# Kernel optimization log

Measured on AMD Instinct MI355X. Metric: run time of the kernel, lower is better.

## Reference

```python
import jax, jax.numpy as jnp
import numpy as np

B, T, D = 64, 512, 256
K = 8192  # num_embeddings


def setup_inputs() -> dict:
    key = jax.random.key(0)
    k1, k2 = jax.random.split(key)
    inputs = jax.random.normal(k1, (B, T, D), dtype=jnp.float32)
    # nn.Embedding weight init: uniform(-1/K, 1/K)
    emb_weight = jax.random.uniform(k2, (K, D), dtype=jnp.float32, minval=-1.0 / K, maxval=1.0 / K)
    return {"inputs": inputs, "emb_weight": emb_weight}


def reference(inputs, emb_weight):
    d = emb_weight.shape[1]
    flat = inputs.reshape(-1, d)  # [N, D]
    # squared L2 distances to all codes: [N, K]
    distances = (
        jnp.sum(flat * flat, axis=1, keepdims=True)
        + jnp.sum(emb_weight * emb_weight, axis=1)
        - 2.0 * jnp.matmul(flat, emb_weight.T)
    )
    encoding_indices = jnp.argmin(distances, axis=1)  # [N]
    # one-hot @ codebook == direct gather of nearest code
    quantized = emb_weight[encoding_indices].reshape(inputs.shape)
    e_latent_loss = jnp.mean((jax.lax.stop_gradient(quantized) - inputs) ** 2)
    q_latent_loss = jnp.mean((quantized - jax.lax.stop_gradient(inputs)) ** 2)
    loss = q_latent_loss + e_latent_loss
    # straight-through estimator
    quantized_st = inputs + jax.lax.stop_gradient(quantized - inputs)
    return quantized_st, loss, encoding_indices.reshape(inputs.shape[0], -1)
```

## Files before the change

kernel.cpp:

```cpp
#include <hip/hip_runtime.h>

#define N_ROWS 32768
#define DIM 256
#define N_CODES 8192
#define OUT_Q 8388608
#define OUT_LOSS 8388608
#define OUT_IDX 8388609
#define FLAG_GAP 7e-5f
#define GAP3 1e-4f
#define CAND_CAP 262144

#define WS_AROW 0
#define WS_IDX  131072
#define WS_LIST 262144
#define WS_CNT  393216
#define WS_S1   393472
#define WS_KEYS 524544
#define WS_PART 524544
#define WS_EIMG 1048576

typedef __attribute__((ext_vector_type(8))) short short8x;
typedef __attribute__((ext_vector_type(4))) float f32x4;
typedef unsigned long long u64;
#define AS1 __attribute__((address_space(1)))
#define AS3 __attribute__((address_space(3)))

__device__ __forceinline__ u64 umin64(u64 a, u64 b) { return a < b ? a : b; }
__device__ __forceinline__ unsigned fkey(float f) {
    unsigned b = __float_as_uint(f);
    return b ^ (unsigned)(((int)b >> 31) | 0x80000000);
}
__device__ __forceinline__ float fkeyinv(unsigned u) {
    unsigned b = (u >> 31) ? (u ^ 0x80000000u) : ~u;
    return __uint_as_float(b);
}
__device__ __forceinline__ unsigned short bf16rne(float f) {
    unsigned u = __float_as_uint(f);
    return (unsigned short)((u + 0x7fff + ((u >> 16) & 1)) >> 16);
}
__device__ __forceinline__ void gload16(const void* g, void* l) {
    __builtin_amdgcn_global_load_lds((const AS1 unsigned int*)g, (AS3 unsigned int*)l, 16, 0, 0);
}
__device__ __forceinline__ void triple_merge(u64& k1, u64& k2, u64& k3, u64 o1, u64 o2, u64 o3) {
    bool c = o1 < k1;
    u64 A1 = c ? o1 : k1, A2 = c ? o2 : k2, A3 = c ? o3 : k3;
    u64 B1 = c ? k1 : o1, B2 = c ? k2 : o2;
    bool d = B1 < A2;
    k1 = A1;
    k2 = d ? B1 : A2;
    k3 = d ? umin64(A2, B2) : umin64(A3, B1);
}

__global__ void vq_prepE(const float* __restrict__ E, char* __restrict__ Eimg) {
    int t = blockIdx.x * 256 + threadIdx.x;
    int cb = t >> 10;
    int u = t & 1023;
    int w = u >> 7, v = u & 127;
    int sub = v >> 5, c = (v >> 4) & 1, l15 = v & 15;
    int tile = cb >> 3, S = cb & 7;
    const float* src = E + (size_t)(tile * 256 + w * 32 + c * 16 + l15) * DIM + S * 32 + sub * 8;
    unsigned short h[8], l[8];
#pragma unroll
    for (int j = 0; j < 8; ++j) {
        float vv = src[j];
        h[j] = bf16rne(vv);
        float hf = __uint_as_float((unsigned)h[j] << 16);
        l[j] = bf16rne(vv - hf);
    }
    short8x H, L;
#pragma unroll
    for (int j = 0; j < 8; ++j) { H[j] = (short)h[j]; L[j] = (short)l[j]; }
    char* dst = Eimg + (size_t)cb * 32768 + w * 4096 + sub * 512 + c * 256 + l15 * 16;
    *(short8x*)dst = H;
    *(short8x*)(dst + 2048) = L;
}

__global__ void vq_rowA(const float* __restrict__ X, float* __restrict__ Arow) {
    int row = blockIdx.x * 4 + (threadIdx.x >> 6);
    int lane = threadIdx.x & 63;
    const float4 v = *((const float4*)(X + (size_t)row * DIM + lane * 4));
    double s = (double)v.x * v.x + (double)v.y * v.y + (double)v.z * v.z + (double)v.w * v.w;
#pragma unroll
    for (int m = 1; m < 64; m <<= 1) s += __shfl_xor(s, m, 64);
    if (lane == 0) Arow[row] = (float)s;
}

template <int MODE>
__global__ __launch_bounds__(512, 1) void vq_scan(
    const float* __restrict__ X, const char* __restrict__ Eimg,
    const float* __restrict__ Arow, int* __restrict__ ws_idx,
    int* __restrict__ flaglist, int* __restrict__ flagcnt,
    u64* __restrict__ keybuf, float* __restrict__ s1buf,
    unsigned* __restrict__ cand, int* __restrict__ candcnt,
    int* __restrict__ list2, int* __restrict__ cnt2) {
    __shared__ alignas(16) unsigned short Xs[32768];
    __shared__ alignas(16) unsigned short Eb[32768];
    __shared__ int rows_s[64];

    const int tid = threadIdx.x;
    const int lane = tid & 63, wv = tid >> 6;
    const int l15 = lane & 15, sub = lane >> 4;

    const int cnt = (MODE == 1) ? *flagcnt : 0;
    const int ntasks = (MODE == 1) ? ((cnt + 63) >> 6) * 16 : 0;

    char* const ebase = (char*)Eb + wv * 4096;
    const char* const eimgw = Eimg + wv * 4096;

    float r1v[4][4], r2v[4][4], r3v[4][4];
    int c1v[4][4], c2v[4][4];
    if constexpr (MODE == 0) {
#pragma unroll
        for (int f = 0; f < 4; ++f)
#pragma unroll
            for (int g = 0; g < 4; ++g) {
                r1v[f][g] = 3.4e38f; r2v[f][g] = 3.4e38f; r3v[f][g] = 3.4e38f;
                c1v[f][g] = 0; c2v[f][g] = 0;
            }
    }

    int task = blockIdx.x;
    while (true) {
        int t0, t1, r0;
        if constexpr (MODE == 1) {
            if (task >= ntasks) break;
            int grp = task >> 4;
            int rng = task & 15;
            t0 = rng * 2; t1 = t0 + 2;
            r0 = 0;
            __syncthreads();
            if (tid < 64) {
                int s = grp * 64 + tid;
                rows_s[tid] = flaglist[s < cnt ? s : cnt - 1];
            }
            __syncthreads();
        } else {
            t0 = 0; t1 = 32;
            r0 = blockIdx.x * 64;
        }
        const int cend = t1 * 8;

        {
            const int ci = t0 * 8;
            const char* src = eimgw + (size_t)ci * 32768 + lane * 16;
            char* dst = ebase + (ci & 1) * 32768;
#pragma unroll
            for (int i = 0; i < 4; ++i) gload16(src + i * 1024, dst + i * 1024);
        }
#pragma unroll
        for (int i = 0; i < 4; ++i) {
            int ci = tid + i * 512;
            int q = ci >> 6, r = ci & 63;
            int grow = (MODE == 1) ? rows_s[r] : r0 + r;
            const float* src = X + (size_t)grow * DIM + q * 8;
            unsigned short h[8], l[8];
#pragma unroll
            for (int j = 0; j < 8; ++j) {
                float v = src[j];
                h[j] = bf16rne(v);
                float hf = __uint_as_float((unsigned)h[j] << 16);
                l[j] = bf16rne(v - hf);
            }
            short8x H, L;
#pragma unroll
            for (int j = 0; j < 8; ++j) { H[j] = (short)h[j]; L[j] = (short)l[j]; }
            *(short8x*)((char*)Xs + q * 1024 + r * 16) = H;
            *(short8x*)((char*)Xs + 32768 + q * 1024 + r * 16) = L;
        }

        float A_r[4][4], s1v[4][4];
        int rid[4][4];
#pragma unroll
        for (int f = 0; f < 4; ++f)
#pragma unroll
            for (int g = 0; g < 4; ++g) {
                int rr = (MODE == 1) ? rows_s[f * 16 + sub * 4 + g] : r0 + f * 16 + sub * 4 + g;
                A_r[f][g] = Arow[rr];
                if constexpr (MODE == 1) { s1v[f][g] = s1buf[rr]; rid[f][g] = rr; }
            }

        __syncthreads();

        for (int t = t0; t < t1; ++t) {
            f32x4 acc[4][2];
#pragma unroll
            for (int f = 0; f < 4; ++f)
#pragma unroll
                for (int c = 0; c < 2; ++c) acc[f][c] = (f32x4){0.f, 0.f, 0.f, 0.f};

#pragma unroll
            for (int S = 0; S < 8; ++S) {
                const int ci = t * 8 + S;
                if (ci + 1 < cend) {
                    const char* src = eimgw + (size_t)(ci + 1) * 32768 + lane * 16;
                    char* dst = ebase + ((ci + 1) & 1) * 32768;
#pragma unroll
                    for (int i = 0; i < 4; ++i) gload16(src + i * 1024, dst + i * 1024);
                    __builtin_amdgcn_sched_barrier(0);
                    asm volatile("s_waitcnt vmcnt(4)" ::: "memory");
                } else {
                    asm volatile("s_waitcnt vmcnt(0)" ::: "memory");
                }
                __builtin_amdgcn_sched_barrier(0);

                const char* xb = (const char*)Xs;
                const char* eb = ebase + (ci & 1) * 32768;
                short8x ah[4], al[4], ehh[2], ell[2];
#pragma unroll
                for (int f = 0; f < 4; ++f) {
                    int off = (S * 4 + sub) * 1024 + f * 256 + l15 * 16;
                    ah[f] = *(const short8x*)(xb + off);
                    al[f] = *(const short8x*)(xb + 32768 + off);
                }
#pragma unroll
                for (int c = 0; c < 2; ++c) {
                    int off = sub * 512 + c * 256 + l15 * 16;
                    ehh[c] = *(const short8x*)(eb + off);
                    ell[c] = *(const short8x*)(eb + 2048 + off);
                }
#pragma unroll
                for (int f = 0; f < 4; ++f)
#pragma unroll
                    for (int c = 0; c < 2; ++c) {
                        f32x4 a = acc[f][c];
                        a = __builtin_amdgcn_mfma_f32_16x16x32_bf16(al[f], ehh[c], a, 0, 0, 0);
                        a = __builtin_amdgcn_mfma_f32_16x16x32_bf16(ah[f], ell[c], a, 0, 0, 0);
                        a = __builtin_amdgcn_mfma_f32_16x16x32_bf16(ah[f], ehh[c], a, 0, 0, 0);
                        acc[f][c] = a;
                    }
            }

            const int cbase = t * 256 + wv * 32 + l15;
            if constexpr (MODE == 0) {
#pragma unroll
                for (int f = 0; f < 4; ++f)
#pragma unroll
                    for (int g = 0; g < 4; ++g) {
                        float v0 = fmaf(-2.0f, acc[f][0][g], A_r[f][g]);
                        float v1 = fmaf(-2.0f, acc[f][1][g], A_r[f][g]);
                        bool sw = v1 < v0;
                        float lo = sw ? v1 : v0, hi = sw ? v0 : v1;
                        int ilo = sw ? cbase + 16 : cbase;
                        int ihi = sw ? cbase : cbase + 16;
                        bool cond = lo < r1v[f][g];
                        float A2 = cond ? hi : r2v[f][g];
                        float A3 = cond ? 3.4e38f : r3v[f][g];
                        float B1 = cond ? r1v[f][g] : lo;
                        float B2 = cond ? r2v[f][g] : hi;
                        int iA2 = cond ? ihi : c2v[f][g];
                        int iB1 = cond ? c1v[f][g] : ilo;
                        r1v[f][g] = cond ? lo : r1v[f][g];
                        c1v[f][g] = cond ? ilo : c1v[f][g];
                        bool d = B1 < A2;
                        r2v[f][g] = d ? B1 : A2;
                        c2v[f][g] = d ? iB1 : iA2;
                        r3v[f][g] = d ? fminf(A2, B2) : fminf(A3, B1);
                    }
            } else {
#pragma unroll
                for (int f = 0; f < 4; ++f)
#pragma unroll
                    for (int g = 0; g < 4; ++g) {
                        float thr = s1v[f][g] + FLAG_GAP;
#pragma unroll
                        for (int c = 0; c < 2; ++c) {
                            float v = fmaf(-2.0f, acc[f][c][g], A_r[f][g]);
                            if (v <= thr) {
                                int slot = atomicAdd(candcnt, 1);
                                if (slot < CAND_CAP)
                                    cand[slot] = ((unsigned)rid[f][g] << 13) |
                                                 (unsigned)(cbase + c * 16);
                            }
                        }
                    }
            }
        }

        if constexpr (MODE == 0) break;
        else task += gridDim.x;
    }

    if constexpr (MODE == 0) {
        __syncthreads();
        u64* red = (u64*)Xs;
#pragma unroll
        for (int f = 0; f < 4; ++f)
#pragma unroll
            for (int g = 0; g < 4; ++g) {
                u64 k1 = ((u64)fkey(r1v[f][g]) << 32) | (unsigned)c1v[f][g];
                u64 k2 = ((u64)fkey(r2v[f][g]) << 32) | (unsigned)c2v[f][g];
                u64 k3 = ((u64)fkey(r3v[f][g]) << 32) | 0x1fffu;
#pragma unroll
                for (int m = 1; m < 16; m <<= 1) {
                    u64 o1 = __shfl_xor(k1, m, 64);
                    u64 o2 = __shfl_xor(k2, m, 64);
                    u64 o3 = __shfl_xor(k3, m, 64);
                    triple_merge(k1, k2, k3, o1, o2, o3);
                }
                if (l15 == 0) {
                    int row64 = f * 16 + sub * 4 + g;
                    red[(wv * 64 + row64) * 3 + 0] = k1;
                    red[(wv * 64 + row64) * 3 + 1] = k2;
                    red[(wv * 64 + row64) * 3 + 2] = k3;
                }
            }
        __syncthreads();
        if (tid < 64) {
            u64 K1 = red[tid * 3 + 0], K2 = red[tid * 3 + 1], K3 = red[tid * 3 + 2];
#pragma unroll
            for (int w = 1; w < 8; ++w) {
                triple_merge(K1, K2, K3,
                             red[(w * 64 + tid) * 3 + 0],
                             red[(w * 64 + tid) * 3 + 1],
                             red[(w * 64 + tid) * 3 + 2]);
            }
            int r = blockIdx.x * 64 + tid;
            ws_idx[r] = (int)(unsigned)(K1 & 0xffffffffull);
            float s1 = fkeyinv((unsigned)(K1 >> 32));
            float s2 = fkeyinv((unsigned)(K2 >> 32));
            float s3 = fkeyinv((unsigned)(K3 >> 32));
            s1buf[r] = s1;
            if (s2 - s1 < FLAG_GAP) {
                keybuf[r] = ~0ull;
                flaglist[atomicAdd(flagcnt, 1)] = r;
                int cs = atomicAdd(candcnt, 2);
                if (cs + 1 < CAND_CAP) {
                    cand[cs]     = ((unsigned)r << 13) | (unsigned)(K1 & 8191ull);
                    cand[cs + 1] = ((unsigned)r << 13) | (unsigned)(K2 & 8191ull);
                }
                if (s3 - s1 <= GAP3) list2[atomicAdd(cnt2, 1)] = r;
            }
        }
    }
}

__global__ void vq_refine_cand(const float* __restrict__ X, const float* __restrict__ E,
                               const float* __restrict__ Arow, u64* __restrict__ keybuf,
                               const unsigned* __restrict__ cand,
                               const int* __restrict__ candcnt) {
    int cnt2 = *candcnt;
    cnt2 = cnt2 < CAND_CAP ? cnt2 : CAND_CAP;
    const int gw = (blockIdx.x * 256 + threadIdx.x) >> 6;
    const int nw = gridDim.x * 4;
    const int lane = threadIdx.x & 63;
    for (int i = gw; i < cnt2; i += nw) {
        unsigned p = cand[i];
        int row = (int)(p >> 13), code = (int)(p & 8191);
        float4 xv = *(const float4*)(X + (size_t)row * DIM + lane * 4);
        float4 ev = *(const float4*)(E + (size_t)code * DIM + lane * 4);
        double s = (double)xv.x * ev.x + (double)xv.y * ev.y +
                   (double)xv.z * ev.z + (double)xv.w * ev.w;
#pragma unroll
        for (int m = 1; m < 64; m <<= 1) s += __shfl_xor(s, m, 64);
        if (lane == 0) {
            float m32 = (float)s;
            float scr = fmaf(-2.0f, m32, Arow[row]);
            u64 key = ((u64)fkey(scr) << 32) | (unsigned)code;
            atomicMin(keybuf + row, key);
        }
    }
}

__global__ void vq_apply(const u64* __restrict__ keybuf, const int* __restrict__ flaglist,
                         const int* __restrict__ flagcnt, int* __restrict__ ws_idx) {
    int s = blockIdx.x * 256 + threadIdx.x;
    if (s < *flagcnt) {
        int r = flaglist[s];
        u64 k = keybuf[r];
        if (k != ~0ull) ws_idx[r] = (int)(unsigned)(k & 0xffffffffull);
    }
}

__global__ void vq_out(const float* __restrict__ X, const float* __restrict__ E,
                       const int* __restrict__ ws_idx, float* __restrict__ out,
                       float* __restrict__ partials) {
    const int r = (blockIdx.x * 256 + threadIdx.x) >> 6;
    const int lane = threadIdx.x & 63;
    int idx = ws_idx[r];
    idx = idx < 0 ? 0 : (idx > N_CODES - 1 ? N_CODES - 1 : idx);
    float4 e = *((const float4*)(E + (size_t)idx * DIM + lane * 4));
    float4 x = *((const float4*)(X + (size_t)r * DIM + lane * 4));
    float dx = e.x - x.x, dy = e.y - x.y, dz = e.z - x.z, dw = e.w - x.w;
    float4 o;
    o.x = x.x + dx; o.y = x.y + dy; o.z = x.z + dz; o.w = x.w + dw;
    *((float4*)(out + (size_t)r * DIM + lane * 4)) = o;
    float s = dx * dx + dy * dy + dz * dz + dw * dw;
#pragma unroll
    for (int m = 1; m < 64; m <<= 1) s += __shfl_xor(s, m, 64);
    if (lane == 0) {
        partials[r] = s;
        out[OUT_IDX + r] = (float)idx;
    }
}

__global__ void vq_loss(const float* __restrict__ partials, float* __restrict__ out) {
    __shared__ double sred[4];
    double s = 0.0;
    for (int i = threadIdx.x; i < N_ROWS; i += 256) s += (double)partials[i];
#pragma unroll
    for (int m = 1; m < 64; m <<= 1) s += __shfl_xor(s, m, 64);
    if ((threadIdx.x & 63) == 0) sred[threadIdx.x >> 6] = s;
    __syncthreads();
    if (threadIdx.x == 0) {
        double t = sred[0] + sred[1] + sred[2] + sred[3];
        out[OUT_LOSS] = (float)(2.0 * t / (double)OUT_Q);
    }
}

extern "C" void kernel_launch(void* const* d_in, const int* in_sizes, int n_in,
                              void* d_out, int out_size, void* d_ws, size_t ws_size,
                              hipStream_t stream) {
    const float* X = (const float*)d_in[0];
    const float* E = (const float*)d_in[1];
    float* out = (float*)d_out;
    char* ws = (char*)d_ws;

    float* Arow = (float*)(ws + WS_AROW);
    int* idx = (int*)(ws + WS_IDX);
    int* list = (int*)(ws + WS_LIST);
    int* cnt = (int*)(ws + WS_CNT);
    int* cnt2 = (int*)(ws + WS_CNT + 8);
    int* ccnt = (int*)(ws + WS_CNT + 16);
    float* s1buf = (float*)(ws + WS_S1);
    u64* keys = (u64*)(ws + WS_KEYS);
    float* part = (float*)(ws + WS_PART);
    char* eimg = (ws_size >= (size_t)(WS_EIMG + 8 * 1024 * 1024)) ? (ws + WS_EIMG) : (char*)d_out;
    unsigned* cand = (unsigned*)((char*)d_out + (16 << 20));
    int* list2 = (int*)((char*)d_out + (17 << 20));

    hipMemsetAsync(ws + WS_CNT, 0, 32, stream);
    vq_prepE<<<1024, 256, 0, stream>>>(E, eimg);
    vq_rowA<<<N_ROWS / 4, 256, 0, stream>>>(X, Arow);
    vq_scan<0><<<N_ROWS / 64, 512, 0, stream>>>(X, eimg, Arow, idx, list, cnt, keys, s1buf,
                                                cand, ccnt, list2, cnt2);
    vq_scan<1><<<512, 512, 0, stream>>>(X, eimg, Arow, idx, list2, cnt2, keys, s1buf,
                                        cand, ccnt, list2, cnt2);
    vq_refine_cand<<<1024, 256, 0, stream>>>(X, E, Arow, keys, cand, ccnt);
    vq_apply<<<128, 256, 0, stream>>>(keys, list, cnt, idx);
    vq_out<<<N_ROWS / 4, 256, 0, stream>>>(X, E, idx, out, part);
    vq_loss<<<1, 256, 0, stream>>>(part, out);
}
```

Measured before the change: 500.0 us.

## Load codebook fragments directly into registers instead of staging through LDS

Re-lays out the precomputed bf16 hi/lo codebook image so each lane's MFMA B-operand fragment is contiguous. The scan kernel then loads those fragments straight from global memory into registers, prefetching one chunk ahead, instead of using global_load_lds into a double-buffered LDS tile. This removes the 64KB LDS buffer, the LDS reads of E and the explicit vmcnt waits. In exchange it depends on the compiler's own waitcnt placement, and the added unroll-1 pragmas may add loop overhead and limit scheduling.

```diff
diff --git a/kernel.cpp b/kernel.cpp
--- a/kernel.cpp
+++ b/kernel.cpp
@@ -22,8 +22,6 @@
 typedef __attribute__((ext_vector_type(8))) short short8x;
 typedef __attribute__((ext_vector_type(4))) float f32x4;
 typedef unsigned long long u64;
-#define AS1 __attribute__((address_space(1)))
-#define AS3 __attribute__((address_space(3)))
 
 __device__ __forceinline__ u64 umin64(u64 a, u64 b) { return a < b ? a : b; }
 __device__ __forceinline__ unsigned fkey(float f) {
@@ -37,9 +35,6 @@
 __device__ __forceinline__ unsigned short bf16rne(float f) {
     unsigned u = __float_as_uint(f);
     return (unsigned short)((u + 0x7fff + ((u >> 16) & 1)) >> 16);
-}
-__device__ __forceinline__ void gload16(const void* g, void* l) {
-    __builtin_amdgcn_global_load_lds((const AS1 unsigned int*)g, (AS3 unsigned int*)l, 16, 0, 0);
 }
 __device__ __forceinline__ void triple_merge(u64& k1, u64& k2, u64& k3, u64 o1, u64 o2, u64 o3) {
     bool c = o1 < k1;
@@ -53,12 +48,15 @@
 
 __global__ void vq_prepE(const float* __restrict__ E, char* __restrict__ Eimg) {
     int t = blockIdx.x * 256 + threadIdx.x;
-    int cb = t >> 10;
+    int ci = t >> 10;
     int u = t & 1023;
-    int w = u >> 7, v = u & 127;
-    int sub = v >> 5, c = (v >> 4) & 1, l15 = v & 15;
-    int tile = cb >> 3, S = cb & 7;
-    const float* src = E + (size_t)(tile * 256 + w * 32 + c * 16 + l15) * DIM + S * 32 + sub * 8;
+    int wv = u >> 7;
+    int v = u & 127;
+    int c = v >> 6, lane = v & 63;
+    int tile = ci >> 3, S = ci & 7;
+    int code = tile * 256 + wv * 32 + c * 16 + (lane & 15);
+    int k0 = S * 32 + (lane >> 4) * 8;
+    const float* src = E + (size_t)code * DIM + k0;
     unsigned short h[8], l[8];
 #pragma unroll
     for (int j = 0; j < 8; ++j) {
@@ -70,7 +68,7 @@
     short8x H, L;
 #pragma unroll
     for (int j = 0; j < 8; ++j) { H[j] = (short)h[j]; L[j] = (short)l[j]; }
-    char* dst = Eimg + (size_t)cb * 32768 + w * 4096 + sub * 512 + c * 256 + l15 * 16;
+    char* dst = Eimg + (size_t)ci * 32768 + wv * 4096 + c * 1024 + lane * 16;
     *(short8x*)dst = H;
     *(short8x*)(dst + 2048) = L;
 }
@@ -94,7 +92,6 @@
     unsigned* __restrict__ cand, int* __restrict__ candcnt,
     int* __restrict__ list2, int* __restrict__ cnt2) {
     __shared__ alignas(16) unsigned short Xs[32768];
-    __shared__ alignas(16) unsigned short Eb[32768];
     __shared__ int rows_s[64];
 
     const int tid = threadIdx.x;
@@ -104,8 +101,7 @@
     const int cnt = (MODE == 1) ? *flagcnt : 0;
     const int ntasks = (MODE == 1) ? ((cnt + 63) >> 6) * 16 : 0;
 
-    char* const ebase = (char*)Eb + wv * 4096;
-    const char* const eimgw = Eimg + wv * 4096;
+    const char* const eimgw = Eimg + wv * 4096 + lane * 16;
 
     float r1v[4][4], r2v[4][4], r3v[4][4];
     int c1v[4][4], c2v[4][4];
@@ -140,12 +136,13 @@
         }
         const int cend = t1 * 8;
 
+        short8x cu0, cu1, cu2, cu3;
         {
-            const int ci = t0 * 8;
-            const char* src = eimgw + (size_t)ci * 32768 + lane * 16;
-            char* dst = ebase + (ci & 1) * 32768;
-#pragma unroll
-            for (int i = 0; i < 4; ++i) gload16(src + i * 1024, dst + i * 1024);
+            const char* p = eimgw + (size_t)(t0 * 8) * 32768;
+            cu0 = *(const short8x*)p;
+            cu1 = *(const short8x*)(p + 1024);
+            cu2 = *(const short8x*)(p + 2048);
+            cu3 = *(const short8x*)(p + 3072);
         }
 #pragma unroll
         for (int i = 0; i < 4; ++i) {
@@ -181,6 +178,7 @@
 
         __syncthreads();
 
+#pragma unroll 1
         for (int t = t0; t < t1; ++t) {
             f32x4 acc[4][2];
 #pragma unroll
@@ -188,24 +186,18 @@
 #pragma unroll
                 for (int c = 0; c < 2; ++c) acc[f][c] = (f32x4){0.f, 0.f, 0.f, 0.f};
 
-#pragma unroll
+#pragma unroll 1
             for (int S = 0; S < 8; ++S) {
                 const int ci = t * 8 + S;
-                if (ci + 1 < cend) {
-                    const char* src = eimgw + (size_t)(ci + 1) * 32768 + lane * 16;
-                    char* dst = ebase + ((ci + 1) & 1) * 32768;
-#pragma unroll
-                    for (int i = 0; i < 4; ++i) gload16(src + i * 1024, dst + i * 1024);
-                    __builtin_amdgcn_sched_barrier(0);
-                    asm volatile("s_waitcnt vmcnt(4)" ::: "memory");
-                } else {
-                    asm volatile("s_waitcnt vmcnt(0)" ::: "memory");
-                }
-                __builtin_amdgcn_sched_barrier(0);
+                const int cin = (ci + 1 < cend) ? ci + 1 : ci;
+                const char* p = eimgw + (size_t)cin * 32768;
+                short8x pn0 = *(const short8x*)p;
+                short8x pn1 = *(const short8x*)(p + 1024);
+                short8x pn2 = *(const short8x*)(p + 2048);
+                short8x pn3 = *(const short8x*)(p + 3072);
 
                 const char* xb = (const char*)Xs;
-                const char* eb = ebase + (ci & 1) * 32768;
-                short8x ah[4], al[4], ehh[2], ell[2];
+                short8x ah[4], al[4];
 #pragma unroll
                 for (int f = 0; f < 4; ++f) {
                     int off = (S * 4 + sub) * 1024 + f * 256 + l15 * 16;
@@ -213,21 +205,19 @@
                     al[f] = *(const short8x*)(xb + 32768 + off);
                 }
 #pragma unroll
-                for (int c = 0; c < 2; ++c) {
-                    int off = sub * 512 + c * 256 + l15 * 16;
-                    ehh[c] = *(const short8x*)(eb + off);
-                    ell[c] = *(const short8x*)(eb + 2048 + off);
+                for (int f = 0; f < 4; ++f) {
+                    f32x4 a0 = acc[f][0];
+                    a0 = __builtin_amdgcn_mfma_f32_16x16x32_bf16(al[f], cu0, a0, 0, 0, 0);
+                    a0 = __builtin_amdgcn_mfma_f32_16x16x32_bf16(ah[f], cu2, a0, 0, 0, 0);
+                    a0 = __builtin_amdgcn_mfma_f32_16x16x32_bf16(ah[f], cu0, a0, 0, 0, 0);
+                    acc[f][0] = a0;
+                    f32x4 a1 = acc[f][1];
+                    a1 = __builtin_amdgcn_mfma_f32_16x16x32_bf16(al[f], cu1, a1, 0, 0, 0);
+                    a1 = __builtin_amdgcn_mfma_f32_16x16x32_bf16(ah[f], cu3, a1, 0, 0, 0);
+                    a1 = __builtin_amdgcn_mfma_f32_16x16x32_bf16(ah[f], cu1, a1, 0, 0, 0);
+                    acc[f][1] = a1;
                 }
-#pragma unroll
-                for (int f = 0; f < 4; ++f)
-#pragma unroll
-                    for (int c = 0; c < 2; ++c) {
-                        f32x4 a = acc[f][c];
-                        a = __builtin_amdgcn_mfma_f32_16x16x32_bf16(al[f], ehh[c], a, 0, 0, 0);
-                        a = __builtin_amdgcn_mfma_f32_16x16x32_bf16(ah[f], ell[c], a, 0, 0, 0);
-                        a = __builtin_amdgcn_mfma_f32_16x16x32_bf16(ah[f], ehh[c], a, 0, 0, 0);
-                        acc[f][c] = a;
-                    }
+                cu0 = pn0; cu1 = pn1; cu2 = pn2; cu3 = pn3;
             }
 
             const int cbase = t * 256 + wv * 32 + l15;
```

Result: no change. 492.6 us (-1.5%).
